# Optimization experiments

Measured on AMD Instinct MI355X. Metric: run time of the kernel, lower is better.

The kernel has to match this reference:

```python
import jax, jax.numpy as jnp
import numpy as np

U, S, D = 4096, 8192, 32
NUM_REGIONS = 128
GA = 0.1


def setup_inputs() -> dict:
    key = jax.random.key(0)
    k1, k2, k3, k4, k5, k6 = jax.random.split(key, 6)
    user_emb = jax.random.normal(k1, (U, D), dtype=jnp.float32) * 0.01
    item_emb = jax.random.normal(k2, (S, D), dtype=jnp.float32) * 0.01
    train_mask = jax.random.randint(k3, (U, S), 0, 2, dtype=jnp.int32)
    true_qos = jax.random.normal(k4, (U, S), dtype=jnp.float32)
    us_lossweight = jax.random.uniform(k5, (U, S), dtype=jnp.float32)
    region_index = jax.random.randint(k6, (U,), 0, NUM_REGIONS, dtype=jnp.int32)
    return {
        "user_emb": user_emb,
        "item_emb": item_emb,
        "train_mask": train_mask,
        "true_qos": true_qos,
        "us_lossweight": us_lossweight,
        "region_index": region_index,
    }


def _region_loss(user_emb, region_index):
    # per-region sums and counts via a single segment reduction
    sums = jax.ops.segment_sum(user_emb, region_index, num_segments=NUM_REGIONS)  # [R, D]
    counts = jax.ops.segment_sum(jnp.ones((user_emb.shape[0],), dtype=user_emb.dtype),
                                 region_index, num_segments=NUM_REGIONS)  # [R]
    cnt = counts[region_index]                      # [U]
    loo_mean = (sums[region_index] - user_emb) / jnp.maximum(cnt - 1.0, 1.0)[:, None]
    dev = jnp.abs(user_emb - loo_mean)              # [U, D]
    # regions with a single user are skipped in the original loop
    valid = (cnt > 1.0)[:, None]
    return jnp.sum(jnp.where(valid, dev, 0.0))


def reference(user_emb, item_emb, train_mask, true_qos, us_lossweight, region_index):
    pre_qos = (user_emb @ item_emb.T) * train_mask.astype(user_emb.dtype)  # [U, S]
    mse = (pre_qos - true_qos) ** 2
    loss = jnp.sum(us_lossweight * mse)
    regionloss = _region_loss(user_emb, region_index)
    return loss + GA * regionloss
```

## Files before the change

kernel.cpp:

```cpp
#include <hip/hip_runtime.h>

#define U 4096
#define S 8192
#define D 32
#define NUM_REGIONS 128
#define GA 0.1f

#define WU 16
#define WI 1024
#define THREADS 256
#define LCAP 256

typedef short          frag8_t __attribute__((ext_vector_type(8)));
typedef unsigned short u16x8_t __attribute__((ext_vector_type(8)));
typedef float          fx4_t   __attribute__((ext_vector_type(4)));

__device__ inline void split8(const float4 a, const float4 b, frag8_t& hi, frag8_t& lo) {
    u16x8_t h, l;
    float vv[8] = {a.x, a.y, a.z, a.w, b.x, b.y, b.z, b.w};
    #pragma unroll
    for (int j = 0; j < 8; j++) {
        unsigned bits = __float_as_uint(vv[j]);
        h[j] = (unsigned short)(bits >> 16);
        float r = vv[j] - __uint_as_float(bits & 0xFFFF0000u);
        l[j] = (unsigned short)(__float_as_uint(r) >> 16);
    }
    hi = __builtin_bit_cast(frag8_t, h);
    lo = __builtin_bit_cast(frag8_t, l);
}


__global__ __launch_bounds__(THREADS) void fused_kernel(
    const float* __restrict__ user_emb,
    const float* __restrict__ item_emb,
    const int* __restrict__ train_mask,
    const float* __restrict__ true_qos,
    const float* __restrict__ us_lossweight,
    const int* __restrict__ region_index,
    float* __restrict__ loss_accum,
    float* __restrict__ rl_accum) {
    __shared__ float wp[THREADS / 64];
    __shared__ int   ulist[LCAP];
    __shared__ int   ucnt;
    __shared__ float part[8][D];
    __shared__ float redsum[D];

    const int lane = threadIdx.x & 63;
    const int wid  = threadIdx.x >> 6;
    const int n16  = lane & 15;
    const int g    = lane >> 4;
    const int kb   = g * 8;

    const int ub      = blockIdx.x * WU;
    const int it_base = blockIdx.y * WI + wid * 256;

    frag8_t uh, ul;
    {
        const float* up = user_emb + (ub + n16) * D + kb;
        split8(*(const float4*)up, *(const float4*)(up + 4), uh, ul);
    }

    const unsigned soff = (unsigned)(ub + n16) * S + it_base + g * 4;
    const int*   mp  = train_mask    + soff;
    const float* qp  = true_qos      + soff;
    const float* wtp = us_lossweight + soff;
    const float* ip  = item_emb + (it_base + n16) * D + kb;

    float acc = 0.0f;
    for (int t = 0; t < 16; t++) {
        int4   m4 = *(const int4*)(mp + t * 16);
        float4 q4 = *(const float4*)(qp + t * 16);
        float4 w4 = *(const float4*)(wtp + t * 16);

        frag8_t ih, il;
        split8(*(const float4*)(ip + t * 16 * D),
               *(const float4*)(ip + t * 16 * D + 4), ih, il);

        fx4_t c = {0.0f, 0.0f, 0.0f, 0.0f};
        c = __builtin_amdgcn_mfma_f32_16x16x32_bf16(ih, uh, c, 0, 0, 0);
        c = __builtin_amdgcn_mfma_f32_16x16x32_bf16(il, uh, c, 0, 0, 0);
        c = __builtin_amdgcn_mfma_f32_16x16x32_bf16(ih, ul, c, 0, 0, 0);

        float p0 = c[0] * (float)m4.x; float e0 = p0 - q4.x; acc += w4.x * e0 * e0;
        float p1 = c[1] * (float)m4.y; float e1 = p1 - q4.y; acc += w4.y * e1 * e1;
        float p2 = c[2] * (float)m4.z; float e2 = p2 - q4.z; acc += w4.z * e2 * e2;
        float p3 = c[3] * (float)m4.w; float e3 = p3 - q4.w; acc += w4.w * e3 * e3;
    }

    #pragma unroll
    for (int off = 32; off > 0; off >>= 1) acc += __shfl_down(acc, off, 64);
    if (lane == 0) wp[wid] = acc;
    __syncthreads();
    if (threadIdx.x == 0)
        atomicAdd(loss_accum, wp[0] + wp[1] + wp[2] + wp[3]);

    if (blockIdx.y != 0 || blockIdx.x >= NUM_REGIONS) return;
    const int r = blockIdx.x;

    __syncthreads();
    if (threadIdx.x == 0) ucnt = 0;
    __syncthreads();

    for (int u = threadIdx.x; u < U; u += 256) {
        if (region_index[u] == r) {
            int p = atomicAdd(&ucnt, 1);
            if (p < LCAP) ulist[p] = u;
        }
    }
    __syncthreads();

    const int n = min(ucnt, LCAP);
    const int d = threadIdx.x & (D - 1);
    const int w8 = threadIdx.x >> 5;

    float psum = 0.0f;
    for (int i = w8; i < n; i += 8)
        psum += user_emb[ulist[i] * D + d];
    part[w8][d] = psum;
    __syncthreads();
    if (w8 == 0) {
        float sum = 0.0f;
        #pragma unroll
        for (int i = 0; i < 8; i++) sum += part[i][d];
        redsum[d] = sum;
    }
    __syncthreads();

    float racc = 0.0f;
    if (n > 1) {
        const float inv = 1.0f / (float)(n - 1);
        const float sd = redsum[d];
        for (int i = w8; i < n; i += 8) {
            float e = user_emb[ulist[i] * D + d];
            racc += fabsf(e - (sd - e) * inv);
        }
    }

    #pragma unroll
    for (int off = 32; off > 0; off >>= 1) racc += __shfl_down(racc, off, 64);
    if (lane == 0) wp[wid] = racc;
    __syncthreads();
    if (threadIdx.x == 0)
        atomicAdd(rl_accum, wp[0] + wp[1] + wp[2] + wp[3]);
}

__global__ void finalize_kernel(const float* __restrict__ loss_acc,
                                const float* __restrict__ rl_acc,
                                float* __restrict__ out) {
    out[0] = loss_acc[0] + GA * rl_acc[0];
}

extern "C" void kernel_launch(void* const* d_in, const int* in_sizes, int n_in,
                              void* d_out, int out_size, void* d_ws, size_t ws_size,
                              hipStream_t stream) {
    const float* user_emb      = (const float*)d_in[0];
    const float* item_emb      = (const float*)d_in[1];
    const int*   train_mask    = (const int*)d_in[2];
    const float* true_qos      = (const float*)d_in[3];
    const float* us_lossweight = (const float*)d_in[4];
    const int*   region_index  = (const int*)d_in[5];
    float* out = (float*)d_out;

    float* ws       = (float*)d_ws;
    float* loss_acc = ws;
    float* rl_acc   = ws + 1;
    hipMemsetAsync(d_ws, 0, 2 * sizeof(float), stream);

    dim3 grid(U / WU, S / WI);
    fused_kernel<<<grid, THREADS, 0, stream>>>(
        user_emb, item_emb, train_mask, true_qos, us_lossweight, region_index,
        loss_acc, rl_acc);

    finalize_kernel<<<1, 1, 0, stream>>>(loss_acc, rl_acc, out);
}
```

Measured before the change: 377.7 us.

## Double-buffer global loads into LDS via direct global_load_lds pipelining

Replaces the direct global vector loads of mask, qos, weight and item embeddings with asynchronous global-to-LDS copies, double-buffered per wave, so the next tile's loads overlap the current tile's MFMA and loss math. The per-block item width is halved and the grid doubled, giving more blocks and shorter per-wave loops. This adds 40KB of LDS per block, which can lower occupancy, and relies on hand-written vmcnt waits matching the five loads issued per stage.

Result: no change. 374.9 us (-0.7%).

```diff
diff --git a/kernel.cpp b/kernel.cpp
--- a/kernel.cpp
+++ b/kernel.cpp
@@ -7,7 +7,8 @@
 #define GA 0.1f
 
 #define WU 16
-#define WI 1024
+#define WI 512
+#define NT 8
 #define THREADS 256
 #define LCAP 256
 
@@ -27,6 +28,12 @@
     }
     hi = __builtin_bit_cast(frag8_t, h);
     lo = __builtin_bit_cast(frag8_t, l);
+}
+
+__device__ __forceinline__ void stage16(const void* g, void* l) {
+    __builtin_amdgcn_global_load_lds(
+        (const __attribute__((address_space(1))) unsigned*)g,
+        (__attribute__((address_space(3))) unsigned*)l, 16, 0, 0);
 }
 
 
@@ -39,6 +46,7 @@
     const int* __restrict__ region_index,
     float* __restrict__ loss_accum,
     float* __restrict__ rl_accum) {
+    __shared__ __align__(16) char stg[4][2][5][1024];
     __shared__ float wp[THREADS / 64];
     __shared__ int   ulist[LCAP];
     __shared__ int   ucnt;
@@ -52,7 +60,7 @@
     const int kb   = g * 8;
 
     const int ub      = blockIdx.x * WU;
-    const int it_base = blockIdx.y * WI + wid * 256;
+    const int it_base = blockIdx.y * WI + wid * (WI / 4);
 
     frag8_t uh, ul;
     {
@@ -66,16 +74,37 @@
     const float* wtp = us_lossweight + soff;
     const float* ip  = item_emb + (it_base + n16) * D + kb;
 
+#define ISSUE(t, slot)                                                \
+    do {                                                              \
+        stage16(mp + (t) * 16,           &stg[wid][slot][0][0]);      \
+        stage16(qp + (t) * 16,           &stg[wid][slot][1][0]);      \
+        stage16(wtp + (t) * 16,          &stg[wid][slot][2][0]);      \
+        stage16(ip + (t) * 16 * D,       &stg[wid][slot][3][0]);      \
+        stage16(ip + (t) * 16 * D + 4,   &stg[wid][slot][4][0]);      \
+    } while (0)
+
     float acc = 0.0f;
-    for (int t = 0; t < 16; t++) {
-        int4   m4 = *(const int4*)(mp + t * 16);
-        float4 q4 = *(const float4*)(qp + t * 16);
-        float4 w4 = *(const float4*)(wtp + t * 16);
+
+    ISSUE(0, 0);
+    #pragma unroll
+    for (int t = 0; t < NT; t++) {
+        const int slot = t & 1;
+        if (t + 1 < NT) {
+            ISSUE(t + 1, (t + 1) & 1);
+            asm volatile("s_waitcnt vmcnt(5)" ::: "memory");
+        } else {
+            asm volatile("s_waitcnt vmcnt(0)" ::: "memory");
+        }
+        __builtin_amdgcn_sched_barrier(0);
+
+        int4   m4 = *(const int4*)  &stg[wid][slot][0][lane * 16];
+        float4 q4 = *(const float4*)&stg[wid][slot][1][lane * 16];
+        float4 w4 = *(const float4*)&stg[wid][slot][2][lane * 16];
+        float4 ia = *(const float4*)&stg[wid][slot][3][lane * 16];
+        float4 ib = *(const float4*)&stg[wid][slot][4][lane * 16];
 
         frag8_t ih, il;
-        split8(*(const float4*)(ip + t * 16 * D),
-               *(const float4*)(ip + t * 16 * D + 4), ih, il);
-
+        split8(ia, ib, ih, il);
         fx4_t c = {0.0f, 0.0f, 0.0f, 0.0f};
         c = __builtin_amdgcn_mfma_f32_16x16x32_bf16(ih, uh, c, 0, 0, 0);
         c = __builtin_amdgcn_mfma_f32_16x16x32_bf16(il, uh, c, 0, 0, 0);
@@ -86,6 +115,7 @@
         float p2 = c[2] * (float)m4.z; float e2 = p2 - q4.z; acc += w4.z * e2 * e2;
         float p3 = c[3] * (float)m4.w; float e3 = p3 - q4.w; acc += w4.w * e3 * e3;
     }
+#undef ISSUE
 
     #pragma unroll
     for (int off = 32; off > 0; off >>= 1) acc += __shfl_down(acc, off, 64);
```
